# Kernel tuning notes

Hardware: AMD Instinct MI355X
Metric: run time of the kernel (lower is better)

Reference implementation:

```python
import jax, jax.numpy as jnp
import numpy as np

B, OBS, H, A, E = 131072, 194, 64, 5, 3  # batch, obs dim, hidden, max_action_dim, n event types


def setup_inputs() -> dict:
    key = jax.random.key(0)
    ks = jax.random.split(key, 16)
    s = lambda k, shape, std=0.1: (jax.random.normal(k, shape, dtype=jnp.float32) * std)
    return {
        "x": jax.random.normal(ks[0], (B, OBS), dtype=jnp.float32),
        "action": jax.random.randint(ks[1], (B,), 0, A),
        "W1": s(ks[2], (OBS, H)), "b1": jnp.zeros((H,), jnp.float32),
        "W2": s(ks[3], (H, H)),   "b2": jnp.zeros((H,), jnp.float32),
        "Wh": s(ks[4], (E, H, A), 0.01), "bh": jnp.zeros((E, A), jnp.float32),
        "Wc1": s(ks[5], (OBS, H)), "bc1": jnp.zeros((H,), jnp.float32),
        "Wc2": s(ks[6], (H, H)),   "bc2": jnp.zeros((H,), jnp.float32),
        "Wc3": s(ks[7], (H, 1)),   "bc3": jnp.zeros((1,), jnp.float32),
    }


def reference(x, action, W1, b1, W2, b2, Wh, bh, Wc1, bc1, Wc2, bc2, Wc3, bc3):
    # shared trunk
    feat = jnp.tanh(jnp.tanh(x @ W1 + b1) @ W2 + b2)          # [B, H]
    # route each sample to one of E heads via argmax of first 3 obs dims
    ev = jnp.argmax(x[:, :E], axis=1)                          # [B] int
    all_logits = jnp.einsum('bh,eha->bea', feat, Wh) + bh      # [B, E, A]
    logits = jnp.take_along_axis(
        all_logits, jnp.broadcast_to(ev[:, None, None], (x.shape[0], 1, A)), axis=1
    )[:, 0]                                                    # [B, A]
    logp_all = jax.nn.log_softmax(logits, axis=-1)             # [B, A]
    logp = jnp.take_along_axis(logp_all, action[:, None], axis=1)[:, 0]  # [B]
    entropy = -jnp.sum(jnp.exp(logp_all) * logp_all, axis=-1)  # [B]
    # critic
    value = jnp.tanh(jnp.tanh(x @ Wc1 + bc1) @ Wc2 + bc2) @ Wc3 + bc3    # [B, 1]
    return action, logp, entropy, value
```

## Files before the change

### kernel.cpp

```cpp
#include <hip/hip_runtime.h>
#include <hip/hip_bf16.h>

constexpr int Bt    = 131072;
constexpr int OBS   = 194;
constexpr int NT    = 512;
constexpr int RPB   = 512;
constexpr int ITERS = 4;
constexpr int RS    = 72;
constexpr int LS    = 18;

constexpr int W1B_S  = 0;
constexpr int WC1B_S = 14336;
constexpr int W2B_S  = 28672;
constexpr int WC2B_S = 36864;
constexpr int WHB_S  = 45056;

constexpr int L_W1  = 0;
constexpr int L_WC1 = 28672;
constexpr int L_W2  = 57344;
constexpr int L_WC2 = 73728;
constexpr int L_WH  = 90112;
constexpr int L_HA  = 92160;
constexpr int L_LG  = 129024;
constexpr int L_VB  = 133632;
constexpr int L_TOT = 134144;

typedef short bf8   __attribute__((ext_vector_type(8)));
typedef float f32x4 __attribute__((ext_vector_type(4)));
typedef unsigned int u32;

__device__ __forceinline__ short f2bs(float f) {
    union { __hip_bfloat16 h; short s; } u;
    u.h = __float2bfloat16(f);
    return u.s;
}
__device__ __forceinline__ float bs2f(short s) {
    union { short s; __hip_bfloat16 h; } u;
    u.s = s;
    return __bfloat162float(u.h);
}
__device__ __forceinline__ u32 pk2(float a, float b) {
    union { __hip_bfloat162 h; u32 u; } r;
    r.h = __float22bfloat162_rn(float2{a, b});
    return r.u;
}
__device__ __forceinline__ float fast_tanh(float v) {
    v = fminf(fmaxf(v, -15.f), 15.f);
    float e = __expf(2.f * v);
    return (e - 1.f) * __builtin_amdgcn_rcpf(e + 1.f);
}
__device__ __forceinline__ void dma16(const void* g, void* s) {
    __builtin_amdgcn_global_load_lds(
        (const __attribute__((address_space(1))) u32*)g,
        (__attribute__((address_space(3))) u32*)s, 16, 0, 0);
}

__global__ void __launch_bounds__(256) prep(
    const float* __restrict__ W1, const float* __restrict__ b1,
    const float* __restrict__ W2, const float* __restrict__ Wh,
    const float* __restrict__ Wc1, const float* __restrict__ bc1,
    const float* __restrict__ Wc2, const float* __restrict__ Wc3,
    short* __restrict__ ws)
{
    const int gid = blockIdx.x * 256 + threadIdx.x;
    const int gsz = gridDim.x * 256;

    for (int i = gid; i < 14336; i += gsz) {
        int j = i & 7, l = (i >> 3) & 63, nt = (i >> 9) & 3, kb = i >> 11;
        int k = kb * 32 + ((l >> 4) << 3) + j;
        int n = nt * 16 + (l & 15);
        short v1 = 0, v2 = 0;
        if (k < OBS) {
            v1 = f2bs(W1[k * 64 + n]);
            v2 = f2bs(Wc1[k * 64 + n]);
        } else if (k == OBS) {
            v1 = f2bs(b1[n]);
            v2 = f2bs(bc1[n]);
        }
        ws[W1B_S + i]  = v1;
        ws[WC1B_S + i] = v2;
    }
    for (int i = gid; i < 8192; i += gsz) {
        int j = i & 7, l = (i >> 3) & 63, nt = (i >> 9) & 3, kb = i >> 11;
        int s = kb * 32 + ((l >> 4) << 3) + j;
        int kp = (s & 3) * 16 + (s >> 2);
        int n = nt * 16 + (l & 15);
        ws[W2B_S + i]  = f2bs(W2[kp * 64 + n]);
        ws[WC2B_S + i] = f2bs(Wc2[kp * 64 + n]);
    }
    for (int i = gid; i < 1024; i += gsz) {
        int j = i & 7, l = (i >> 3) & 63, kb = i >> 9;
        int s = kb * 32 + ((l >> 4) << 3) + j;
        int kp = (s & 3) * 16 + (s >> 2);
        int cc = l & 15;
        float v;
        if (cc == 15) v = Wc3[kp];
        else { int e = cc / 5, a = cc - 5 * e; v = Wh[(e * 64 + kp) * 5 + a]; }
        ws[WHB_S + i] = f2bs(v);
    }
}

__global__ void __launch_bounds__(NT, 2) fused_ac(
    const float* __restrict__ x, const int* __restrict__ act_in,
    const float* __restrict__ b2, const float* __restrict__ bc2,
    const float* __restrict__ bh, const float* __restrict__ bc3,
    const short* __restrict__ ws,
    float* __restrict__ out)
{
    __shared__ __align__(16) char smem[L_TOT];

    const int t    = threadIdx.x;
    const int w    = t >> 6;
    const int l    = t & 63;
    const int q    = l >> 4;
    const int c    = l & 15;
    const int base = blockIdx.x * RPB;

    #pragma unroll
    for (int i = 0; i < 12; ++i) {
        int idx = i * NT + t;
        if (idx < 5760)
            dma16(((const char*)ws) + idx * 16, smem + idx * 16);
    }

    float b2v[4], bc2v[4];
    #pragma unroll
    for (int nt = 0; nt < 4; ++nt) {
        b2v[nt]  = b2[nt * 16 + c];
        bc2v[nt] = bc2[nt * 16 + c];
    }
    float bhv = (c < 15) ? bh[c] : bc3[0];

    float2 raw[24]; float2 rt6;
    auto loadraw = [&](int gm2) {
        const float* xr = x + (size_t)gm2 * OBS;
        #pragma unroll
        for (int kb = 0; kb < 6; ++kb) {
            const float2* p = reinterpret_cast<const float2*>(xr + kb * 32 + q * 8);
            raw[kb * 4 + 0] = p[0]; raw[kb * 4 + 1] = p[1];
            raw[kb * 4 + 2] = p[2]; raw[kb * 4 + 3] = p[3];
        }
        rt6 = float2{0.f, 0.f};
        if (q == 0) rt6 = *reinterpret_cast<const float2*>(xr + 192);
    };
    union AF { u32 u[4]; bf8 v; } af[7];
    int ev = 0;
    auto packaf = [&]() {
        #pragma unroll
        for (int kb = 0; kb < 6; ++kb) {
            af[kb].u[0] = pk2(raw[kb * 4 + 0].x, raw[kb * 4 + 0].y);
            af[kb].u[1] = pk2(raw[kb * 4 + 1].x, raw[kb * 4 + 1].y);
            af[kb].u[2] = pk2(raw[kb * 4 + 2].x, raw[kb * 4 + 2].y);
            af[kb].u[3] = pk2(raw[kb * 4 + 3].x, raw[kb * 4 + 3].y);
        }
        af[6].u[0] = 0; af[6].u[1] = 0; af[6].u[2] = 0; af[6].u[3] = 0;
        if (q == 0) {
            af[6].u[0] = pk2(rt6.x, rt6.y);
            af[6].u[1] = pk2(1.0f, 0.0f);
        }
        ev = 0;
        float bbest = raw[0].x;
        if (raw[0].y > bbest) { bbest = raw[0].y; ev = 1; }
        if (raw[1].x > bbest) { ev = 2; }
    };

    loadraw(base + w * 16 + c);

    __syncthreads();

    packaf();

    const bf8* fW1L  = reinterpret_cast<const bf8*>(smem + L_W1);
    const bf8* fWc1L = reinterpret_cast<const bf8*>(smem + L_WC1);
    const bf8* fW2L  = reinterpret_cast<const bf8*>(smem + L_W2);
    const bf8* fWc2L = reinterpret_cast<const bf8*>(smem + L_WC2);
    const bf8* fWhL  = reinterpret_cast<const bf8*>(smem + L_WH);
    short* ha = reinterpret_cast<short*>(smem + L_HA + w * 4608);
    short* hc = ha + 2304 / 2;
    short* lw = reinterpret_cast<short*>(smem + L_LG + w * 576);
    float* vb = reinterpret_cast<float*>(smem + L_VB + w * 64);

    #pragma unroll 1
    for (int i = 0; i < ITERS; ++i) {
        const int gm = base + i * 128 + w * 16 + c;
        int act = 0;
        if (l < 16) act = act_in[gm];
        const int evc = ev;

        if (i + 1 < ITERS) loadraw(base + (i + 1) * 128 + w * 16 + c);

        f32x4 aa[4], ac[4];
        #pragma unroll
        for (int nt = 0; nt < 4; ++nt) {
            aa[nt] = f32x4{0.f, 0.f, 0.f, 0.f};
            ac[nt] = f32x4{0.f, 0.f, 0.f, 0.f};
        }
        #pragma unroll
        for (int kb = 0; kb < 7; ++kb) {
            bf8 a = af[kb].v;
            #pragma unroll
            for (int nt = 0; nt < 4; ++nt) {
                aa[nt] = __builtin_amdgcn_mfma_f32_16x16x32_bf16(a, fW1L [(kb * 4 + nt) * 64 + l], aa[nt], 0, 0, 0);
                ac[nt] = __builtin_amdgcn_mfma_f32_16x16x32_bf16(a, fWc1L[(kb * 4 + nt) * 64 + l], ac[nt], 0, 0, 0);
            }
        }
        #pragma unroll
        for (int r = 0; r < 4; ++r) {
            uint2 pa, pc;
            pa.x = pk2(fast_tanh(aa[0][r]), fast_tanh(aa[1][r]));
            pa.y = pk2(fast_tanh(aa[2][r]), fast_tanh(aa[3][r]));
            pc.x = pk2(fast_tanh(ac[0][r]), fast_tanh(ac[1][r]));
            pc.y = pk2(fast_tanh(ac[2][r]), fast_tanh(ac[3][r]));
            *reinterpret_cast<uint2*>(&ha[(q * 4 + r) * RS + 4 * c]) = pa;
            *reinterpret_cast<uint2*>(&hc[(q * 4 + r) * RS + 4 * c]) = pc;
        }

        #pragma unroll
        for (int nt = 0; nt < 4; ++nt) {
            aa[nt] = f32x4{b2v[nt], b2v[nt], b2v[nt], b2v[nt]};
            ac[nt] = f32x4{bc2v[nt], bc2v[nt], bc2v[nt], bc2v[nt]};
        }
        #pragma unroll
        for (int kb = 0; kb < 2; ++kb) {
            bf8 xa = *reinterpret_cast<const bf8*>(&ha[c * RS + kb * 32 + q * 8]);
            bf8 xc = *reinterpret_cast<const bf8*>(&hc[c * RS + kb * 32 + q * 8]);
            #pragma unroll
            for (int nt = 0; nt < 4; ++nt) {
                aa[nt] = __builtin_amdgcn_mfma_f32_16x16x32_bf16(xa, fW2L [(kb * 4 + nt) * 64 + l], aa[nt], 0, 0, 0);
                ac[nt] = __builtin_amdgcn_mfma_f32_16x16x32_bf16(xc, fWc2L[(kb * 4 + nt) * 64 + l], ac[nt], 0, 0, 0);
            }
        }
        #pragma unroll
        for (int r = 0; r < 4; ++r) {
            uint2 pa, pc;
            pa.x = pk2(fast_tanh(aa[0][r]), fast_tanh(aa[1][r]));
            pa.y = pk2(fast_tanh(aa[2][r]), fast_tanh(aa[3][r]));
            pc.x = pk2(fast_tanh(ac[0][r]), fast_tanh(ac[1][r]));
            pc.y = pk2(fast_tanh(ac[2][r]), fast_tanh(ac[3][r]));
            *reinterpret_cast<uint2*>(&ha[(q * 4 + r) * RS + 4 * c]) = pa;
            *reinterpret_cast<uint2*>(&hc[(q * 4 + r) * RS + 4 * c]) = pc;
        }

        {
            f32x4 lg = f32x4{bhv, bhv, bhv, bhv};
            f32x4 vv = f32x4{bhv, bhv, bhv, bhv};
            #pragma unroll
            for (int kb = 0; kb < 2; ++kb) {
                bf8 bw = fWhL[kb * 64 + l];
                bf8 fa = *reinterpret_cast<const bf8*>(&ha[c * RS + kb * 32 + q * 8]);
                bf8 fc = *reinterpret_cast<const bf8*>(&hc[c * RS + kb * 32 + q * 8]);
                lg = __builtin_amdgcn_mfma_f32_16x16x32_bf16(fa, bw, lg, 0, 0, 0);
                vv = __builtin_amdgcn_mfma_f32_16x16x32_bf16(fc, bw, vv, 0, 0, 0);
            }
            #pragma unroll
            for (int r = 0; r < 4; ++r)
                lw[(q * 4 + r) * LS + c] = f2bs(lg[r]);
            if (c == 15) {
                #pragma unroll
                for (int r = 0; r < 4; ++r)
                    vb[q * 4 + r] = vv[r];
            }
        }

        if (l < 16) {
            float lg[5];
            #pragma unroll
            for (int a = 0; a < 5; ++a)
                lg[a] = bs2f(lw[c * LS + evc * 5 + a]);
            float mx = lg[0];
            #pragma unroll
            for (int a = 1; a < 5; ++a) mx = fmaxf(mx, lg[a]);
            float se = 0.f;
            #pragma unroll
            for (int a = 0; a < 5; ++a) se += __expf(lg[a] - mx);
            float lse = __logf(se) + mx;
            float lsel = lg[0];
            #pragma unroll
            for (int a = 1; a < 5; ++a) lsel = (act == a) ? lg[a] : lsel;
            float ent = 0.f;
            #pragma unroll
            for (int a = 0; a < 5; ++a) { float lp = lg[a] - lse; ent -= __expf(lp) * lp; }

            out[gm]          = (float)act;
            out[Bt + gm]     = lsel - lse;
            out[2 * Bt + gm] = ent;
            out[3 * Bt + gm] = vb[c];
        }

        if (i + 1 < ITERS) packaf();
    }
}

extern "C" void kernel_launch(void* const* d_in, const int* in_sizes, int n_in,
                              void* d_out, int out_size, void* d_ws, size_t ws_size,
                              hipStream_t stream) {
    const float* x   = (const float*)d_in[0];
    const int*   act = (const int*)  d_in[1];
    const float* W1  = (const float*)d_in[2];
    const float* b1  = (const float*)d_in[3];
    const float* W2  = (const float*)d_in[4];
    const float* b2  = (const float*)d_in[5];
    const float* Wh  = (const float*)d_in[6];
    const float* bh  = (const float*)d_in[7];
    const float* Wc1 = (const float*)d_in[8];
    const float* bc1 = (const float*)d_in[9];
    const float* Wc2 = (const float*)d_in[10];
    const float* bc2 = (const float*)d_in[11];
    const float* Wc3 = (const float*)d_in[12];
    const float* bc3 = (const float*)d_in[13];
    float* out = (float*)d_out;
    short* ws  = (short*)d_ws;

    hipLaunchKernelGGL(prep, dim3(32), dim3(256), 0, stream,
                       W1, b1, W2, Wh, Wc1, bc1, Wc2, Wc3, ws);
    hipLaunchKernelGGL(fused_ac, dim3(Bt / RPB), dim3(NT), 0, stream,
                       x, act, b2, bc2, bh, bc3, ws, out);
}
```

Baseline: 182.3 us.

## Split fused actor-critic kernel into trunk and head kernels with global staging

Splits the single fused kernel into two. The first kernel streams x tiles into LDS with async DMA, runs the first layer and writes the hidden activations and event ids to a global workspace. The second kernel reads them back and runs the second layer, the heads and the softmax. The goal is to lower LDS pressure per kernel and overlap x loading with compute, at the cost of an extra global round-trip for the hidden states and an additional launch.

```diff
diff --git a/kernel.cpp b/kernel.cpp
--- a/kernel.cpp
+++ b/kernel.cpp
@@ -3,27 +3,14 @@
 
 constexpr int Bt    = 131072;
 constexpr int OBS   = 194;
-constexpr int NT    = 512;
-constexpr int RPB   = 512;
-constexpr int ITERS = 4;
-constexpr int RS    = 72;
-constexpr int LS    = 18;
 
 constexpr int W1B_S  = 0;
 constexpr int WC1B_S = 14336;
 constexpr int W2B_S  = 28672;
 constexpr int WC2B_S = 36864;
 constexpr int WHB_S  = 45056;
-
-constexpr int L_W1  = 0;
-constexpr int L_WC1 = 28672;
-constexpr int L_W2  = 57344;
-constexpr int L_WC2 = 73728;
-constexpr int L_WH  = 90112;
-constexpr int L_HA  = 92160;
-constexpr int L_LG  = 129024;
-constexpr int L_VB  = 133632;
-constexpr int L_TOT = 134144;
+constexpr size_t EVG_B = 98304;
+constexpr size_t HG_S  = 131072;
 
 typedef short bf8   __attribute__((ext_vector_type(8)));
 typedef float f32x4 __attribute__((ext_vector_type(4)));
@@ -100,94 +87,75 @@
     }
 }
 
-__global__ void __launch_bounds__(NT, 2) fused_ac(
-    const float* __restrict__ x, const int* __restrict__ act_in,
-    const float* __restrict__ b2, const float* __restrict__ bc2,
-    const float* __restrict__ bh, const float* __restrict__ bc3,
-    const short* __restrict__ ws,
-    float* __restrict__ out)
+constexpr int P1_XS0 = 57344;
+constexpr int P1_XSS = 12544;
+constexpr int P1_LDS = P1_XS0 + 8 * P1_XSS;
+
+__global__ void __launch_bounds__(512, 2) trunk1(
+    const float* __restrict__ x, const short* __restrict__ ws,
+    short* __restrict__ hG, unsigned char* __restrict__ evG)
 {
-    __shared__ __align__(16) char smem[L_TOT];
-
-    const int t    = threadIdx.x;
-    const int w    = t >> 6;
-    const int l    = t & 63;
-    const int q    = l >> 4;
-    const int c    = l & 15;
-    const int base = blockIdx.x * RPB;
+    __shared__ __align__(16) char smem[P1_LDS];
+    const int t = threadIdx.x;
+    const int w = t >> 6, l = t & 63, q = l >> 4, c = l & 15;
 
     #pragma unroll
-    for (int i = 0; i < 12; ++i) {
-        int idx = i * NT + t;
-        if (idx < 5760)
-            dma16(((const char*)ws) + idx * 16, smem + idx * 16);
-    }
-
-    float b2v[4], bc2v[4];
-    #pragma unroll
-    for (int nt = 0; nt < 4; ++nt) {
-        b2v[nt]  = b2[nt * 16 + c];
-        bc2v[nt] = bc2[nt * 16 + c];
-    }
-    float bhv = (c < 15) ? bh[c] : bc3[0];
-
-    float2 raw[24]; float2 rt6;
-    auto loadraw = [&](int gm2) {
-        const float* xr = x + (size_t)gm2 * OBS;
+    for (int i = 0; i < 7; ++i) {
+        int idx = i * 512 + t;
+        dma16((const char*)ws + idx * 16, smem + idx * 16);
+    }
+
+    char* xs = smem + P1_XS0 + w * P1_XSS;
+    const int t0 = blockIdx.x * 32 + w * 4;
+
+    {
+        const char* src = (const char*)x + (size_t)t0 * 12416;
+        #pragma unroll
+        for (int ch = 0; ch < 12; ++ch)
+            dma16(src + ch * 1024 + l * 16, xs + ch * 1024 + l * 16);
+        if (l < 8) {
+            int4 v = *reinterpret_cast<const int4*>(src + 12288 + l * 16);
+            *reinterpret_cast<int4*>(xs + 12288 + l * 16) = v;
+        }
+    }
+
+    __syncthreads();
+
+    const bf8* fW1L  = reinterpret_cast<const bf8*>(smem);
+    const bf8* fWc1L = reinterpret_cast<const bf8*>(smem + 28672);
+    short* ha = reinterpret_cast<short*>(xs);
+    short* hc = ha + 1152;
+
+    #pragma unroll 1
+    for (int i = 0; i < 4; ++i) {
+        const int tt = t0 + i;
+
+        asm volatile("s_waitcnt vmcnt(0)" ::: "memory");
+        __builtin_amdgcn_sched_barrier(0);
+
+        union AF { u32 u[4]; bf8 v; } af[7];
         #pragma unroll
         for (int kb = 0; kb < 6; ++kb) {
-            const float2* p = reinterpret_cast<const float2*>(xr + kb * 32 + q * 8);
-            raw[kb * 4 + 0] = p[0]; raw[kb * 4 + 1] = p[1];
-            raw[kb * 4 + 2] = p[2]; raw[kb * 4 + 3] = p[3];
-        }
-        rt6 = float2{0.f, 0.f};
-        if (q == 0) rt6 = *reinterpret_cast<const float2*>(xr + 192);
-    };
-    union AF { u32 u[4]; bf8 v; } af[7];
-    int ev = 0;
-    auto packaf = [&]() {
-        #pragma unroll
-        for (int kb = 0; kb < 6; ++kb) {
-            af[kb].u[0] = pk2(raw[kb * 4 + 0].x, raw[kb * 4 + 0].y);
-            af[kb].u[1] = pk2(raw[kb * 4 + 1].x, raw[kb * 4 + 1].y);
-            af[kb].u[2] = pk2(raw[kb * 4 + 2].x, raw[kb * 4 + 2].y);
-            af[kb].u[3] = pk2(raw[kb * 4 + 3].x, raw[kb * 4 + 3].y);
+            #pragma unroll
+            for (int j = 0; j < 4; ++j) {
+                float2 v = *reinterpret_cast<const float2*>(xs + c * 776 + kb * 128 + q * 32 + j * 8);
+                af[kb].u[j] = pk2(v.x, v.y);
+            }
         }
         af[6].u[0] = 0; af[6].u[1] = 0; af[6].u[2] = 0; af[6].u[3] = 0;
         if (q == 0) {
-            af[6].u[0] = pk2(rt6.x, rt6.y);
+            float2 v = *reinterpret_cast<const float2*>(xs + c * 776 + 768);
+            af[6].u[0] = pk2(v.x, v.y);
             af[6].u[1] = pk2(1.0f, 0.0f);
         }
-        ev = 0;
-        float bbest = raw[0].x;
-        if (raw[0].y > bbest) { bbest = raw[0].y; ev = 1; }
-        if (raw[1].x > bbest) { ev = 2; }
-    };
-
-    loadraw(base + w * 16 + c);
-
-    __syncthreads();
-
-    packaf();
-
-    const bf8* fW1L  = reinterpret_cast<const bf8*>(smem + L_W1);
-    const bf8* fWc1L = reinterpret_cast<const bf8*>(smem + L_WC1);
-    const bf8* fW2L  = reinterpret_cast<const bf8*>(smem + L_W2);
-    const bf8* fWc2L = reinterpret_cast<const bf8*>(smem + L_WC2);
-    const bf8* fWhL  = reinterpret_cast<const bf8*>(smem + L_WH);
-    short* ha = reinterpret_cast<short*>(smem + L_HA + w * 4608);
-    short* hc = ha + 2304 / 2;
-    short* lw = reinterpret_cast<short*>(smem + L_LG + w * 576);
-    float* vb = reinterpret_cast<float*>(smem + L_VB + w * 64);
-
-    #pragma unroll 1
-    for (int i = 0; i < ITERS; ++i) {
-        const int gm = base + i * 128 + w * 16 + c;
-        int act = 0;
-        if (l < 16) act = act_in[gm];
-        const int evc = ev;
-
-        if (i + 1 < ITERS) loadraw(base + (i + 1) * 128 + w * 16 + c);
+        if (l < 16) {
+            float2 v01 = *reinterpret_cast<const float2*>(xs + l * 776);
+            float  v2  = *reinterpret_cast<const float*>(xs + l * 776 + 8);
+            int ev = 0; float b = v01.x;
+            if (v01.y > b) { b = v01.y; ev = 1; }
+            if (v2 > b) ev = 2;
+            evG[tt * 16 + l] = (unsigned char)ev;
+        }
 
         f32x4 aa[4], ac[4];
         #pragma unroll
@@ -211,10 +179,86 @@
             pa.y = pk2(fast_tanh(aa[2][r]), fast_tanh(aa[3][r]));
             pc.x = pk2(fast_tanh(ac[0][r]), fast_tanh(ac[1][r]));
             pc.y = pk2(fast_tanh(ac[2][r]), fast_tanh(ac[3][r]));
-            *reinterpret_cast<uint2*>(&ha[(q * 4 + r) * RS + 4 * c]) = pa;
-            *reinterpret_cast<uint2*>(&hc[(q * 4 + r) * RS + 4 * c]) = pc;
-        }
-
+            *reinterpret_cast<uint2*>(&ha[(q * 4 + r) * 72 + 4 * c]) = pa;
+            *reinterpret_cast<uint2*>(&hc[(q * 4 + r) * 72 + 4 * c]) = pc;
+        }
+        #pragma unroll
+        for (int kb = 0; kb < 2; ++kb) {
+            bf8 va = *reinterpret_cast<const bf8*>(&ha[c * 72 + kb * 32 + q * 8]);
+            bf8 vc = *reinterpret_cast<const bf8*>(&hc[c * 72 + kb * 32 + q * 8]);
+            *reinterpret_cast<bf8*>(hG + ((size_t)(tt * 4 + kb)     * 64 + l) * 8) = va;
+            *reinterpret_cast<bf8*>(hG + ((size_t)(tt * 4 + 2 + kb) * 64 + l) * 8) = vc;
+        }
+
+        if (i < 3) {
+            const char* src = (const char*)x + (size_t)(tt + 1) * 12416;
+            #pragma unroll
+            for (int ch = 0; ch < 12; ++ch)
+                dma16(src + ch * 1024 + l * 16, xs + ch * 1024 + l * 16);
+            if (l < 8) {
+                int4 v = *reinterpret_cast<const int4*>(src + 12288 + l * 16);
+                *reinterpret_cast<int4*>(xs + 12288 + l * 16) = v;
+            }
+        }
+    }
+}
+
+constexpr int F2_W   = 34816;
+constexpr int F2_PW  = 5248;
+constexpr int F2_LDS = F2_W + 8 * F2_PW;
+
+__global__ void __launch_bounds__(512, 4) head2(
+    const int* __restrict__ act_in,
+    const float* __restrict__ b2, const float* __restrict__ bc2,
+    const float* __restrict__ bh, const float* __restrict__ bc3,
+    const short* __restrict__ ws,
+    const short* __restrict__ hG, const unsigned char* __restrict__ evG,
+    float* __restrict__ out)
+{
+    __shared__ __align__(16) char smem[F2_LDS];
+    const int t = threadIdx.x;
+    const int w = t >> 6, l = t & 63, q = l >> 4, c = l & 15;
+
+    #pragma unroll
+    for (int i = 0; i < 5; ++i) {
+        int idx = i * 512 + t;
+        if (idx < 2176)
+            dma16((const char*)ws + 57344 + idx * 16, smem + idx * 16);
+    }
+
+    float b2v[4], bc2v[4];
+    #pragma unroll
+    for (int nt = 0; nt < 4; ++nt) {
+        b2v[nt]  = b2[nt * 16 + c];
+        bc2v[nt] = bc2[nt * 16 + c];
+    }
+    float bhv = (c < 15) ? bh[c] : bc3[0];
+
+    __syncthreads();
+
+    const bf8* fW2L  = reinterpret_cast<const bf8*>(smem);
+    const bf8* fWc2L = reinterpret_cast<const bf8*>(smem + 16384);
+    const bf8* fWhL  = reinterpret_cast<const bf8*>(smem + 32768);
+    short* ha = reinterpret_cast<short*>(smem + F2_W + w * F2_PW);
+    short* hc = ha + 1152;
+    short* lw = reinterpret_cast<short*>(smem + F2_W + w * F2_PW + 4608);
+    float* vb = reinterpret_cast<float*>(smem + F2_W + w * F2_PW + 5184);
+
+    #pragma unroll 1
+    for (int i = 0; i < 2; ++i) {
+        const int tt = blockIdx.x * 16 + w * 2 + i;
+        const int gm = tt * 16 + c;
+        int act = 0, evc = 0;
+        if (l < 16) { act = act_in[gm]; evc = evG[gm]; }
+
+        bf8 xa[2], xc[2];
+        #pragma unroll
+        for (int kb = 0; kb < 2; ++kb) {
+            xa[kb] = *reinterpret_cast<const bf8*>(hG + ((size_t)(tt * 4 + kb)     * 64 + l) * 8);
+            xc[kb] = *reinterpret_cast<const bf8*>(hG + ((size_t)(tt * 4 + 2 + kb) * 64 + l) * 8);
+        }
+
+        f32x4 aa[4], ac[4];
         #pragma unroll
         for (int nt = 0; nt < 4; ++nt) {
             aa[nt] = f32x4{b2v[nt], b2v[nt], b2v[nt], b2v[nt]};
@@ -222,12 +266,10 @@
         }
         #pragma unroll
         for (int kb = 0; kb < 2; ++kb) {
-            bf8 xa = *reinterpret_cast<const bf8*>(&ha[c * RS + kb * 32 + q * 8]);
-            bf8 xc = *reinterpret_cast<const bf8*>(&hc[c * RS + kb * 32 + q * 8]);
             #pragma unroll
             for (int nt = 0; nt < 4; ++nt) {
-                aa[nt] = __builtin_amdgcn_mfma_f32_16x16x32_bf16(xa, fW2L [(kb * 4 + nt) * 64 + l], aa[nt], 0, 0, 0);
-                ac[nt] = __builtin_amdgcn_mfma_f32_16x16x32_bf16(xc, fWc2L[(kb * 4 + nt) * 64 + l], ac[nt], 0, 0, 0);
+                aa[nt] = __builtin_amdgcn_mfma_f32_16x16x32_bf16(xa[kb], fW2L [(kb * 4 + nt) * 64 + l], aa[nt], 0, 0, 0);
+                ac[nt] = __builtin_amdgcn_mfma_f32_16x16x32_bf16(xc[kb], fWc2L[(kb * 4 + nt) * 64 + l], ac[nt], 0, 0, 0);
             }
         }
         #pragma unroll
@@ -237,8 +279,8 @@
             pa.y = pk2(fast_tanh(aa[2][r]), fast_tanh(aa[3][r]));
             pc.x = pk2(fast_tanh(ac[0][r]), fast_tanh(ac[1][r]));
             pc.y = pk2(fast_tanh(ac[2][r]), fast_tanh(ac[3][r]));
-            *reinterpret_cast<uint2*>(&ha[(q * 4 + r) * RS + 4 * c]) = pa;
-            *reinterpret_cast<uint2*>(&hc[(q * 4 + r) * RS + 4 * c]) = pc;
+            *reinterpret_cast<uint2*>(&ha[(q * 4 + r) * 72 + 4 * c]) = pa;
+            *reinterpret_cast<uint2*>(&hc[(q * 4 + r) * 72 + 4 * c]) = pc;
         }
 
         {
@@ -247,14 +289,14 @@
             #pragma unroll
             for (int kb = 0; kb < 2; ++kb) {
                 bf8 bw = fWhL[kb * 64 + l];
-                bf8 fa = *reinterpret_cast<const bf8*>(&ha[c * RS + kb * 32 + q * 8]);
-                bf8 fc = *reinterpret_cast<const bf8*>(&hc[c * RS + kb * 32 + q * 8]);
+                bf8 fa = *reinterpret_cast<const bf8*>(&ha[c * 72 + kb * 32 + q * 8]);
+                bf8 fc = *reinterpret_cast<const bf8*>(&hc[c * 72 + kb * 32 + q * 8]);
                 lg = __builtin_amdgcn_mfma_f32_16x16x32_bf16(fa, bw, lg, 0, 0, 0);
                 vv = __builtin_amdgcn_mfma_f32_16x16x32_bf16(fc, bw, vv, 0, 0, 0);
             }
             #pragma unroll
             for (int r = 0; r < 4; ++r)
-                lw[(q * 4 + r) * LS + c] = f2bs(lg[r]);
+                lw[(q * 4 + r) * 18 + c] = f2bs(lg[r]);
             if (c == 15) {
                 #pragma unroll
                 for (int r = 0; r < 4; ++r)
@@ -266,7 +308,7 @@
             float lg[5];
             #pragma unroll
             for (int a = 0; a < 5; ++a)
-                lg[a] = bs2f(lw[c * LS + evc * 5 + a]);
+                lg[a] = bs2f(lw[c * 18 + evc * 5 + a]);
             float mx = lg[0];
             #pragma unroll
             for (int a = 1; a < 5; ++a) mx = fmaxf(mx, lg[a]);
@@ -286,8 +328,6 @@
             out[2 * Bt + gm] = ent;
             out[3 * Bt + gm] = vb[c];
         }
-
-        if (i + 1 < ITERS) packaf();
     }
 }
 
@@ -310,9 +350,13 @@
     const float* bc3 = (const float*)d_in[13];
     float* out = (float*)d_out;
     short* ws  = (short*)d_ws;
+    short* hG  = ws + HG_S;
+    unsigned char* evG = (unsigned char*)d_ws + EVG_B;
 
     hipLaunchKernelGGL(prep, dim3(32), dim3(256), 0, stream,
                        W1, b1, W2, Wh, Wc1, bc1, Wc2, Wc3, ws);
-    hipLaunchKernelGGL(fused_ac, dim3(Bt / RPB), dim3(NT), 0, stream,
-                       x, act, b2, bc2, bh, bc3, ws, out);
-}
+    hipLaunchKernelGGL(trunk1, dim3(256), dim3(512), 0, stream,
+                       x, ws, hG, evG);
+    hipLaunchKernelGGL(head2, dim3(512), dim3(512), 0, stream,
+                       act, b2, bc2, bh, bc3, ws, hG, evG, out);
+}
```

Result: slower. 200.7 us (+10.1%).
